# Optimization experiments

Hardware: AMD Instinct MI355X
Metric: run time of the kernel (lower is better)

The kernel has to match this reference:

```python
import jax, jax.numpy as jnp
import numpy as np

B, S, D = 2, 2048, 1024
H, DH = 16, 64  # num_heads, hidden_dimension (per-head)


def setup_inputs() -> dict:
    key = jax.random.key(0)
    ks = jax.random.split(key, 9)
    s = 1.0 / np.sqrt(D)
    so = 1.0 / np.sqrt(H * DH)
    return {
        "x": jax.random.normal(ks[0], (B, S, D), dtype=jnp.float32),
        "Wq": jax.random.uniform(ks[1], (D, H * DH), jnp.float32, -s, s),
        "bq": jax.random.uniform(ks[2], (H * DH,), jnp.float32, -s, s),
        "Wk": jax.random.uniform(ks[3], (D, H * DH), jnp.float32, -s, s),
        "bk": jax.random.uniform(ks[4], (H * DH,), jnp.float32, -s, s),
        "Wv": jax.random.uniform(ks[5], (D, H * DH), jnp.float32, -s, s),
        "bv": jax.random.uniform(ks[6], (H * DH,), jnp.float32, -s, s),
        "Wo": jax.random.uniform(ks[7], (H * DH, D), jnp.float32, -so, so),
        "bo": jax.random.uniform(ks[8], (D,), jnp.float32, -so, so),
    }


def reference(x, Wq, bq, Wk, bk, Wv, bv, Wo, bo):
    b, s, _ = x.shape
    # project and split heads: [b, h, s, dh]
    q = (x @ Wq + bq).reshape(b, s, H, DH).transpose(0, 2, 1, 3)
    k = (x @ Wk + bk).reshape(b, s, H, DH).transpose(0, 2, 1, 3)
    v = (x @ Wv + bv).reshape(b, s, H, DH).transpose(0, 2, 1, 3)
    scores = jnp.einsum('bhqd,bhkd->bhqk', q, k) / jnp.sqrt(jnp.float32(DH))
    causal = jnp.triu(jnp.ones((s, s), dtype=bool), k=1)
    scores = jnp.where(causal, -jnp.inf, scores)
    weights = jax.nn.softmax(scores, axis=-1)
    out = jnp.einsum('bhqk,bhkd->bhqd', weights, v)
    out = out.transpose(0, 2, 1, 3).reshape(b, s, H * DH)
    return out @ Wo + bo
```

## Files before the change

### kernel.cpp

```cpp
#include <hip/hip_runtime.h>

#define B_  2
#define S_  2048
#define D_  1024
#define H_  16
#define DH_ 64
#define NDH (H_*DH_)
#define BS_ (B_*S_)
#define PER ((size_t)B_*H_*S_*DH_)

typedef __bf16 bf16;
typedef bf16 bf16x8 __attribute__((ext_vector_type(8)));
typedef bf16 bf16x4 __attribute__((ext_vector_type(4)));
typedef float f32x4 __attribute__((ext_vector_type(4)));

#define AS1 __attribute__((address_space(1)))
#define AS3 __attribute__((address_space(3)))
__device__ inline void gld16(const bf16* g, bf16* l) {
    __builtin_amdgcn_global_load_lds((const AS1 void*)g, (AS3 void*)l, 16, 0, 0);
}

__global__ __launch_bounds__(256) void prep(
        const float* __restrict__ x,
        const float* __restrict__ W0, const float* __restrict__ W1,
        const float* __restrict__ W2, const float* __restrict__ W3,
        bf16* __restrict__ xb, bf16* __restrict__ T0, bf16* __restrict__ T1,
        bf16* __restrict__ T2, bf16* __restrict__ T3) {
    __shared__ float T[32][33];
    int bid = blockIdx.x, t = threadIdx.x;
    if (bid < 4096) {
        int i = (bid * 256 + t) * 4;
        float4 v = *(const float4*)(x + i);
        bf16x4 o = { (bf16)v.x, (bf16)v.y, (bf16)v.z, (bf16)v.w };
        *(bf16x4*)(xb + i) = o;
        return;
    }
    int r2 = bid - 4096;
    int z = r2 >> 10, w = r2 & 1023;
    const float* W = (z == 0) ? W0 : (z == 1) ? W1 : (z == 2) ? W2 : W3;
    bf16* Wt = (z == 0) ? T0 : (z == 1) ? T1 : (z == 2) ? T2 : T3;
    int k0 = (w >> 5) * 32, n0 = (w & 31) * 32;
    int r = t >> 3, c = (t & 7) * 4;
    float4 v = *(const float4*)(W + (size_t)(k0 + r) * 1024 + n0 + c);
    T[c + 0][r] = v.x; T[c + 1][r] = v.y; T[c + 2][r] = v.z; T[c + 3][r] = v.w;
    __syncthreads();
    bf16x4 o = { (bf16)T[r][c], (bf16)T[r][c + 1], (bf16)T[r][c + 2], (bf16)T[r][c + 3] };
    *(bf16x4*)(Wt + (size_t)(n0 + r) * 1024 + k0 + c) = o;
}

__global__ __launch_bounds__(256) void qkv_gemm(
        const bf16* __restrict__ A, const bf16* __restrict__ Bt,
        const float* __restrict__ bq, const float* __restrict__ bk,
        const float* __restrict__ bv, bf16* __restrict__ Qout, bf16* __restrict__ Vt) {
    __shared__ __align__(16) bf16 As[128 * 32];
    __shared__ __align__(16) bf16 Bs[128 * 32];
    int tid = threadIdx.x, wave = tid >> 6, lane = tid & 63;
    int quad = lane >> 4, l16 = lane & 15;
    int bm = blockIdx.y * 128, bn = blockIdx.x * 128;
    int wm = (wave >> 1) * 64, wn = (wave & 1) * 64;

    int sr = lane >> 2, sc = (lane & 3) * 8;
    const bf16* Ag0 = A + (size_t)(bm + (wave * 2 + 0) * 16 + sr) * 1024 + sc;
    const bf16* Ag1 = A + (size_t)(bm + (wave * 2 + 1) * 16 + sr) * 1024 + sc;
    const bf16* Bg0 = Bt + (size_t)(bn + (wave * 2 + 0) * 16 + sr) * 1024 + sc;
    const bf16* Bg1 = Bt + (size_t)(bn + (wave * 2 + 1) * 16 + sr) * 1024 + sc;
    bf16* Al0 = &As[(wave * 2 + 0) * 512];
    bf16* Al1 = &As[(wave * 2 + 1) * 512];
    bf16* Bl0 = &Bs[(wave * 2 + 0) * 512];
    bf16* Bl1 = &Bs[(wave * 2 + 1) * 512];

    f32x4 acc[4][4] = {};

    for (int k0 = 0; k0 < 1024; k0 += 32) {
        gld16(Ag0 + k0, Al0);
        gld16(Ag1 + k0, Al1);
        gld16(Bg0 + k0, Bl0);
        gld16(Bg1 + k0, Bl1);
        __syncthreads();
        bf16x8 af[4], bfr[4];
        #pragma unroll
        for (int i = 0; i < 4; ++i)
            af[i] = *(const bf16x8*)&As[(wm + i * 16 + l16) * 32 + quad * 8];
        #pragma unroll
        for (int j = 0; j < 4; ++j)
            bfr[j] = *(const bf16x8*)&Bs[(wn + j * 16 + l16) * 32 + quad * 8];
        #pragma unroll
        for (int i = 0; i < 4; ++i)
          #pragma unroll
          for (int j = 0; j < 4; ++j)
            acc[i][j] = __builtin_amdgcn_mfma_f32_16x16x32_bf16(af[i], bfr[j], acc[i][j], 0, 0, 0);
        __syncthreads();
    }

    #pragma unroll
    for (int i = 0; i < 4; ++i)
      #pragma unroll
      for (int j = 0; j < 4; ++j) {
        int col = bn + wn + j * 16 + l16;
        float bias = (col < 1024) ? bq[col] : (col < 2048) ? bk[col - 1024] : bv[col - 2048];
        int qkv = col >> 10, cw = col & 1023;
        int hh = cw >> 6, d = cw & 63;
        int row0 = bm + wm + i * 16 + quad * 4;
        int bb = row0 >> 11, s0 = row0 & 2047;
        if (qkv < 2) {
            #pragma unroll
            for (int r = 0; r < 4; ++r)
                Qout[(size_t)qkv * PER + (((size_t)bb * H_ + hh) * S_ + s0 + r) * DH_ + d] =
                    (bf16)(acc[i][j][r] + bias);
        } else {
            bf16x4 pack;
            #pragma unroll
            for (int r = 0; r < 4; ++r) pack[r] = (bf16)(acc[i][j][r] + bias);
            *(bf16x4*)&Vt[(((size_t)bb * H_ + hh) * DH_ + d) * S_ + s0] = pack;
        }
      }
}

__global__ __launch_bounds__(256) void gemm128f(
        const bf16* __restrict__ A, const bf16* __restrict__ Bt,
        const float* __restrict__ bias, float* __restrict__ out) {
    __shared__ __align__(16) bf16 As[128 * 32];
    __shared__ __align__(16) bf16 Bs[128 * 32];
    int tid = threadIdx.x, wave = tid >> 6, lane = tid & 63;
    int quad = lane >> 4, l16 = lane & 15;
    int bm = blockIdx.y * 128, bn = blockIdx.x * 128;
    int wm = (wave >> 1) * 64, wn = (wave & 1) * 64;

    int sr = lane >> 2, sc = (lane & 3) * 8;
    const bf16* Ag0 = A + (size_t)(bm + (wave * 2 + 0) * 16 + sr) * 1024 + sc;
    const bf16* Ag1 = A + (size_t)(bm + (wave * 2 + 1) * 16 + sr) * 1024 + sc;
    const bf16* Bg0 = Bt + (size_t)(bn + (wave * 2 + 0) * 16 + sr) * 1024 + sc;
    const bf16* Bg1 = Bt + (size_t)(bn + (wave * 2 + 1) * 16 + sr) * 1024 + sc;
    bf16* Al0 = &As[(wave * 2 + 0) * 512];
    bf16* Al1 = &As[(wave * 2 + 1) * 512];
    bf16* Bl0 = &Bs[(wave * 2 + 0) * 512];
    bf16* Bl1 = &Bs[(wave * 2 + 1) * 512];

    f32x4 acc[4][4] = {};

    for (int k0 = 0; k0 < 1024; k0 += 32) {
        gld16(Ag0 + k0, Al0);
        gld16(Ag1 + k0, Al1);
        gld16(Bg0 + k0, Bl0);
        gld16(Bg1 + k0, Bl1);
        __syncthreads();
        bf16x8 af[4], bfr[4];
        #pragma unroll
        for (int i = 0; i < 4; ++i)
            af[i] = *(const bf16x8*)&As[(wm + i * 16 + l16) * 32 + quad * 8];
        #pragma unroll
        for (int j = 0; j < 4; ++j)
            bfr[j] = *(const bf16x8*)&Bs[(wn + j * 16 + l16) * 32 + quad * 8];
        #pragma unroll
        for (int i = 0; i < 4; ++i)
          #pragma unroll
          for (int j = 0; j < 4; ++j)
            acc[i][j] = __builtin_amdgcn_mfma_f32_16x16x32_bf16(af[i], bfr[j], acc[i][j], 0, 0, 0);
        __syncthreads();
    }

    #pragma unroll
    for (int i = 0; i < 4; ++i)
      #pragma unroll
      for (int j = 0; j < 4; ++j) {
        int col = bn + wn + j * 16 + l16;
        float b = bias[col];
        #pragma unroll
        for (int r = 0; r < 4; ++r) {
            int row = bm + wm + i * 16 + quad * 4 + r;
            out[(size_t)row * 1024 + col] = acc[i][j][r] + b;
        }
      }
}

__global__ __launch_bounds__(256) void flash4(
        const bf16* __restrict__ Q, const bf16* __restrict__ K,
        const bf16* __restrict__ Vt, bf16* __restrict__ O) {
    int bh = blockIdx.x;
    int b = bh >> 4, h = bh & 15;
    int pr = blockIdx.y;
    int tid = threadIdx.x;
    int wave = tid >> 6, lane = tid & 63;
    int quad = lane >> 4, l16 = lane & 15;

    __shared__ __align__(16) char smem[4 * 2 * 16 * 72 * 2];
    bf16 (*P)[2][16][72] = reinterpret_cast<bf16 (*)[2][16][72]>(smem);
    float (*redO)[4][64][4] = reinterpret_cast<float (*)[4][64][4]>(smem);
    __shared__ float redL[4][2][4][4];

    const bf16* Qb = Q + (size_t)bh * S_ * DH_;
    const bf16* Kb = K + (size_t)bh * S_ * DH_;
    const bf16* Vb = Vt + (size_t)bh * DH_ * S_;

    bf16x8 ones;
    #pragma unroll
    for (int j = 0; j < 8; ++j) ones[j] = (l16 == 0) ? (bf16)1.0f : (bf16)0.0f;

    for (int half = 0; half < 2; ++half) {
        int tile = half ? (63 - pr) : pr;
        int q0 = tile * 32;

        bf16x8 qf[2][2];
        #pragma unroll
        for (int s = 0; s < 2; ++s) {
            const bf16* qp = Qb + (size_t)(q0 + s * 16 + l16) * DH_ + quad * 8;
            qf[s][0] = *(const bf16x8*)(qp);
            qf[s][1] = *(const bf16x8*)(qp + 32);
        }

        f32x4 oacc[2][4] = {};
        f32x4 lacc[2] = {};

        int nkt = tile / 2 + 1;
        for (int kt = wave; kt < nkt; kt += 4) {
            int kv0 = kt * 64;
            bf16x8 kf[4][2];
            #pragma unroll
            for (int ns = 0; ns < 4; ++ns) {
                const bf16* kp = Kb + (size_t)(kv0 + ns * 16 + l16) * DH_ + quad * 8;
                kf[ns][0] = *(const bf16x8*)(kp);
                kf[ns][1] = *(const bf16x8*)(kp + 32);
            }
            f32x4 sacc[2][4] = {};
            #pragma unroll
            for (int s = 0; s < 2; ++s)
              #pragma unroll
              for (int ns = 0; ns < 4; ++ns) {
                sacc[s][ns] = __builtin_amdgcn_mfma_f32_16x16x32_bf16(qf[s][0], kf[ns][0], sacc[s][ns], 0, 0, 0);
                sacc[s][ns] = __builtin_amdgcn_mfma_f32_16x16x32_bf16(qf[s][1], kf[ns][1], sacc[s][ns], 0, 0, 0);
              }
            bool diag = (kt == nkt - 1);
            #pragma unroll
            for (int s = 0; s < 2; ++s)
              #pragma unroll
              for (int ns = 0; ns < 4; ++ns)
                #pragma unroll
                for (int r = 0; r < 4; ++r) {
                    float p = __expf(sacc[s][ns][r] * 0.125f);
                    if (diag) {
                        int kv = kv0 + ns * 16 + l16;
                        int qq = q0 + s * 16 + quad * 4 + r;
                        if (kv > qq) p = 0.f;
                    }
                    P[wave][s][quad * 4 + r][ns * 16 + l16] = (bf16)p;
                }
            #pragma unroll
            for (int ks = 0; ks < 2; ++ks) {
                bf16x8 pf0 = *(const bf16x8*)&P[wave][0][l16][ks * 32 + quad * 8];
                bf16x8 pf1 = *(const bf16x8*)&P[wave][1][l16][ks * 32 + quad * 8];
                lacc[0] = __builtin_amdgcn_mfma_f32_16x16x32_bf16(pf0, ones, lacc[0], 0, 0, 0);
                lacc[1] = __builtin_amdgcn_mfma_f32_16x16x32_bf16(pf1, ones, lacc[1], 0, 0, 0);
                #pragma unroll
                for (int ds = 0; ds < 4; ++ds) {
                    bf16x8 vf = *(const bf16x8*)(Vb + (size_t)(ds * 16 + l16) * S_ + kv0 + ks * 32 + quad * 8);
                    oacc[0][ds] = __builtin_amdgcn_mfma_f32_16x16x32_bf16(pf0, vf, oacc[0][ds], 0, 0, 0);
                    oacc[1][ds] = __builtin_amdgcn_mfma_f32_16x16x32_bf16(pf1, vf, oacc[1][ds], 0, 0, 0);
                }
            }
        }

        if (l16 == 0) {
            #pragma unroll
            for (int s = 0; s < 2; ++s)
              #pragma unroll
              for (int r = 0; r < 4; ++r)
                redL[wave][s][quad][r] = lacc[s][r];
        }
        #pragma unroll
        for (int s = 0; s < 2; ++s) {
            __syncthreads();
            #pragma unroll
            for (int ds = 0; ds < 4; ++ds)
                *(f32x4*)&redO[wave][ds][lane][0] = oacc[s][ds];
            __syncthreads();
            f32x4 osum = {};
            #pragma unroll
            for (int w = 0; w < 4; ++w)
                osum += *(const f32x4*)&redO[w][wave][lane][0];
            #pragma unroll
            for (int r = 0; r < 4; ++r) {
                float lsum = redL[0][s][quad][r] + redL[1][s][quad][r]
                           + redL[2][s][quad][r] + redL[3][s][quad][r];
                int qq = q0 + s * 16 + quad * 4 + r;
                O[((size_t)b * S_ + qq) * NDH + h * DH_ + wave * 16 + l16] = (bf16)(osum[r] / lsum);
            }
        }
        __syncthreads();
    }
}

extern "C" void kernel_launch(void* const* d_in, const int* in_sizes, int n_in,
                              void* d_out, int out_size, void* d_ws, size_t ws_size,
                              hipStream_t stream) {
    const float* x  = (const float*)d_in[0];
    const float* Wq = (const float*)d_in[1];
    const float* bq = (const float*)d_in[2];
    const float* Wk = (const float*)d_in[3];
    const float* bk = (const float*)d_in[4];
    const float* Wv = (const float*)d_in[5];
    const float* bv = (const float*)d_in[6];
    const float* Wo = (const float*)d_in[7];
    const float* bo = (const float*)d_in[8];
    float* out = (float*)d_out;

    bf16* ws = (bf16*)d_ws;
    const size_t M1 = (size_t)1024 * 1024;
    bf16* xb    = ws;
    bf16* WqkvT = ws + 4 * M1;
    bf16* WoT   = ws + 7 * M1;
    bf16* Qw    = ws + 8 * M1;
    bf16* Vtw   = ws + 16 * M1;
    bf16* Ow    = ws + 20 * M1;

    prep<<<8192, 256, 0, stream>>>(x, Wq, Wk, Wv, Wo,
                                   xb, WqkvT, WqkvT + M1, WqkvT + 2 * M1, WoT);

    qkv_gemm<<<dim3(3072 / 128, BS_ / 128), 256, 0, stream>>>(xb, WqkvT, bq, bk, bv, Qw, Vtw);

    flash4<<<dim3(B_ * H_, 32), 256, 0, stream>>>(Qw, Qw + PER, Vtw, Ow);

    gemm128f<<<dim3(1024 / 128, BS_ / 128), 256, 0, stream>>>(Ow, WoT, bo, out);
}
```

Before: 220.3 us.

## Software-pipeline flash attention with double-buffered P, fold scale into Q, narrow output GEMM tile

```diff
diff --git a/kernel.cpp b/kernel.cpp
--- a/kernel.cpp
+++ b/kernel.cpp
@@ -13,6 +13,8 @@
 typedef bf16 bf16x8 __attribute__((ext_vector_type(8)));
 typedef bf16 bf16x4 __attribute__((ext_vector_type(4)));
 typedef float f32x4 __attribute__((ext_vector_type(4)));
+
+#define QSCALE 0.18033688011112042f
 
 #define AS1 __attribute__((address_space(1)))
 #define AS3 __attribute__((address_space(3)))
@@ -103,10 +105,11 @@
         int row0 = bm + wm + i * 16 + quad * 4;
         int bb = row0 >> 11, s0 = row0 & 2047;
         if (qkv < 2) {
+            float scl = (qkv == 0) ? QSCALE : 1.0f;
             #pragma unroll
             for (int r = 0; r < 4; ++r)
                 Qout[(size_t)qkv * PER + (((size_t)bb * H_ + hh) * S_ + s0 + r) * DH_ + d] =
-                    (bf16)(acc[i][j][r] + bias);
+                    (bf16)((acc[i][j][r] + bias) * scl);
         } else {
             bf16x4 pack;
             #pragma unroll
@@ -116,45 +119,42 @@
       }
 }
 
-__global__ __launch_bounds__(256) void gemm128f(
+__global__ __launch_bounds__(256) void gemm_proj(
         const bf16* __restrict__ A, const bf16* __restrict__ Bt,
         const float* __restrict__ bias, float* __restrict__ out) {
     __shared__ __align__(16) bf16 As[128 * 32];
-    __shared__ __align__(16) bf16 Bs[128 * 32];
+    __shared__ __align__(16) bf16 Bs[64 * 32];
     int tid = threadIdx.x, wave = tid >> 6, lane = tid & 63;
     int quad = lane >> 4, l16 = lane & 15;
-    int bm = blockIdx.y * 128, bn = blockIdx.x * 128;
-    int wm = (wave >> 1) * 64, wn = (wave & 1) * 64;
+    int bm = blockIdx.y * 128, bn = blockIdx.x * 64;
+    int wm = (wave >> 1) * 64, wn = (wave & 1) * 32;
 
     int sr = lane >> 2, sc = (lane & 3) * 8;
     const bf16* Ag0 = A + (size_t)(bm + (wave * 2 + 0) * 16 + sr) * 1024 + sc;
     const bf16* Ag1 = A + (size_t)(bm + (wave * 2 + 1) * 16 + sr) * 1024 + sc;
-    const bf16* Bg0 = Bt + (size_t)(bn + (wave * 2 + 0) * 16 + sr) * 1024 + sc;
-    const bf16* Bg1 = Bt + (size_t)(bn + (wave * 2 + 1) * 16 + sr) * 1024 + sc;
+    const bf16* Bg0 = Bt + (size_t)(bn + wave * 16 + sr) * 1024 + sc;
     bf16* Al0 = &As[(wave * 2 + 0) * 512];
     bf16* Al1 = &As[(wave * 2 + 1) * 512];
-    bf16* Bl0 = &Bs[(wave * 2 + 0) * 512];
-    bf16* Bl1 = &Bs[(wave * 2 + 1) * 512];
-
-    f32x4 acc[4][4] = {};
+    bf16* Bl0 = &Bs[wave * 512];
+
+    f32x4 acc[4][2] = {};
 
     for (int k0 = 0; k0 < 1024; k0 += 32) {
         gld16(Ag0 + k0, Al0);
         gld16(Ag1 + k0, Al1);
         gld16(Bg0 + k0, Bl0);
-        gld16(Bg1 + k0, Bl1);
-        __syncthreads();
-        bf16x8 af[4], bfr[4];
+        __syncthreads();
+        bf16x8 af[4], bfr[2];
         #pragma unroll
         for (int i = 0; i < 4; ++i)
             af[i] = *(const bf16x8*)&As[(wm + i * 16 + l16) * 32 + quad * 8];
         #pragma unroll
-        for (int j = 0; j < 4; ++j)
+        for (int j = 0; j < 2; ++j)
             bfr[j] = *(const bf16x8*)&Bs[(wn + j * 16 + l16) * 32 + quad * 8];
         #pragma unroll
         for (int i = 0; i < 4; ++i)
           #pragma unroll
-          for (int j = 0; j < 4; ++j)
+          for (int j = 0; j < 2; ++j)
             acc[i][j] = __builtin_amdgcn_mfma_f32_16x16x32_bf16(af[i], bfr[j], acc[i][j], 0, 0, 0);
         __syncthreads();
     }
@@ -162,7 +162,7 @@
     #pragma unroll
     for (int i = 0; i < 4; ++i)
       #pragma unroll
-      for (int j = 0; j < 4; ++j) {
+      for (int j = 0; j < 2; ++j) {
         int col = bn + wn + j * 16 + l16;
         float b = bias[col];
         #pragma unroll
@@ -173,7 +173,7 @@
       }
 }
 
-__global__ __launch_bounds__(256) void flash4(
+__global__ __launch_bounds__(256, 4) void flash5(
         const bf16* __restrict__ Q, const bf16* __restrict__ K,
         const bf16* __restrict__ Vt, bf16* __restrict__ O) {
     int bh = blockIdx.x;
@@ -183,8 +183,8 @@
     int wave = tid >> 6, lane = tid & 63;
     int quad = lane >> 4, l16 = lane & 15;
 
-    __shared__ __align__(16) char smem[4 * 2 * 16 * 72 * 2];
-    bf16 (*P)[2][16][72] = reinterpret_cast<bf16 (*)[2][16][72]>(smem);
+    __shared__ __align__(16) char smem[4 * 2 * 2 * 16 * 72 * 2];
+    bf16 (*P)[2][2][16][72] = reinterpret_cast<bf16 (*)[2][2][16][72]>(smem);
     float (*redO)[4][64][4] = reinterpret_cast<float (*)[4][64][4]>(smem);
     __shared__ float redL[4][2][4][4];
 
@@ -211,43 +211,12 @@
         f32x4 oacc[2][4] = {};
         f32x4 lacc[2] = {};
 
-        int nkt = tile / 2 + 1;
-        for (int kt = wave; kt < nkt; kt += 4) {
-            int kv0 = kt * 64;
-            bf16x8 kf[4][2];
-            #pragma unroll
-            for (int ns = 0; ns < 4; ++ns) {
-                const bf16* kp = Kb + (size_t)(kv0 + ns * 16 + l16) * DH_ + quad * 8;
-                kf[ns][0] = *(const bf16x8*)(kp);
-                kf[ns][1] = *(const bf16x8*)(kp + 32);
-            }
-            f32x4 sacc[2][4] = {};
-            #pragma unroll
-            for (int s = 0; s < 2; ++s)
-              #pragma unroll
-              for (int ns = 0; ns < 4; ++ns) {
-                sacc[s][ns] = __builtin_amdgcn_mfma_f32_16x16x32_bf16(qf[s][0], kf[ns][0], sacc[s][ns], 0, 0, 0);
-                sacc[s][ns] = __builtin_amdgcn_mfma_f32_16x16x32_bf16(qf[s][1], kf[ns][1], sacc[s][ns], 0, 0, 0);
-              }
-            bool diag = (kt == nkt - 1);
-            #pragma unroll
-            for (int s = 0; s < 2; ++s)
-              #pragma unroll
-              for (int ns = 0; ns < 4; ++ns)
-                #pragma unroll
-                for (int r = 0; r < 4; ++r) {
-                    float p = __expf(sacc[s][ns][r] * 0.125f);
-                    if (diag) {
-                        int kv = kv0 + ns * 16 + l16;
-                        int qq = q0 + s * 16 + quad * 4 + r;
-                        if (kv > qq) p = 0.f;
-                    }
-                    P[wave][s][quad * 4 + r][ns * 16 + l16] = (bf16)p;
-                }
+        auto pv_phase = [&](int p, int kv0) {
             #pragma unroll
             for (int ks = 0; ks < 2; ++ks) {
-                bf16x8 pf0 = *(const bf16x8*)&P[wave][0][l16][ks * 32 + quad * 8];
-                bf16x8 pf1 = *(const bf16x8*)&P[wave][1][l16][ks * 32 + quad * 8];
+                bf16x8 pf0 = *(const bf16x8*)&P[wave][p][0][l16][ks * 32 + quad * 8];
+                bf16x8 pf1 = *(const bf16x8*)&P[wave][p][1][l16][ks * 32 + quad * 8];
+                __builtin_amdgcn_s_setprio(1);
                 lacc[0] = __builtin_amdgcn_mfma_f32_16x16x32_bf16(pf0, ones, lacc[0], 0, 0, 0);
                 lacc[1] = __builtin_amdgcn_mfma_f32_16x16x32_bf16(pf1, ones, lacc[1], 0, 0, 0);
                 #pragma unroll
@@ -256,8 +225,55 @@
                     oacc[0][ds] = __builtin_amdgcn_mfma_f32_16x16x32_bf16(pf0, vf, oacc[0][ds], 0, 0, 0);
                     oacc[1][ds] = __builtin_amdgcn_mfma_f32_16x16x32_bf16(pf1, vf, oacc[1][ds], 0, 0, 0);
                 }
+                __builtin_amdgcn_s_setprio(0);
             }
-        }
+        };
+
+        int nkt = tile / 2 + 1;
+        int par = 0, pkv0 = -1;
+        for (int kt = wave; kt < nkt; kt += 4) {
+            int kv0 = kt * 64;
+            bf16x8 kf[4][2];
+            #pragma unroll
+            for (int ns = 0; ns < 4; ++ns) {
+                const bf16* kp = Kb + (size_t)(kv0 + ns * 16 + l16) * DH_ + quad * 8;
+                kf[ns][0] = *(const bf16x8*)(kp);
+                kf[ns][1] = *(const bf16x8*)(kp + 32);
+            }
+            f32x4 sacc[2][4] = {};
+            __builtin_amdgcn_s_setprio(1);
+            #pragma unroll
+            for (int s = 0; s < 2; ++s)
+              #pragma unroll
+              for (int ns = 0; ns < 4; ++ns) {
+                sacc[s][ns] = __builtin_amdgcn_mfma_f32_16x16x32_bf16(kf[ns][0], qf[s][0], sacc[s][ns], 0, 0, 0);
+                sacc[s][ns] = __builtin_amdgcn_mfma_f32_16x16x32_bf16(kf[ns][1], qf[s][1], sacc[s][ns], 0, 0, 0);
+              }
+            __builtin_amdgcn_s_setprio(0);
+
+            if (pkv0 >= 0) pv_phase(par ^ 1, pkv0);
+
+            bool diag = (kt == nkt - 1);
+            #pragma unroll
+            for (int s = 0; s < 2; ++s)
+              #pragma unroll
+              for (int ns = 0; ns < 4; ++ns) {
+                bf16x4 pk;
+                #pragma unroll
+                for (int r = 0; r < 4; ++r) {
+                    float p = __builtin_amdgcn_exp2f(sacc[s][ns][r]);
+                    if (diag) {
+                        int kv = kv0 + ns * 16 + quad * 4 + r;
+                        int qq = q0 + s * 16 + l16;
+                        if (kv > qq) p = 0.f;
+                    }
+                    pk[r] = (bf16)p;
+                }
+                *(bf16x4*)&P[wave][par][s][l16][ns * 16 + quad * 4] = pk;
+              }
+            pkv0 = kv0; par ^= 1;
+        }
+        if (pkv0 >= 0) pv_phase(par ^ 1, pkv0);
 
         if (l16 == 0) {
             #pragma unroll
@@ -317,7 +333,7 @@
 
     qkv_gemm<<<dim3(3072 / 128, BS_ / 128), 256, 0, stream>>>(xb, WqkvT, bq, bk, bv, Qw, Vtw);
 
-    flash4<<<dim3(B_ * H_, 32), 256, 0, stream>>>(Qw, Qw + PER, Vtw, Ow);
-
-    gemm128f<<<dim3(1024 / 128, BS_ / 128), 256, 0, stream>>>(Ow, WoT, bo, out);
-}
+    flash5<<<dim3(B_ * H_, 32), 256, 0, stream>>>(Qw, Qw + PER, Vtw, Ow);
+
+    gemm_proj<<<dim3(1024 / 64, BS_ / 128), 256, 0, stream>>>(Ow, WoT, bo, out);
+}
```

Measured after the change: 243.2 us. +10.4%, slower.
